# Optimization experiments

Measured on AMD Instinct MI355X. Metric: run time of the kernel, lower is better.

Reference implementation:

```python
import jax, jax.numpy as jnp
import numpy as np

WS = 7          # window size
NUM_HEADS = 12

def _relative_position_index(ws):
    # Same construction as the torch module; pure numpy constants.
    coords = np.stack(np.meshgrid(np.arange(ws), np.arange(ws), indexing='ij'))  # [2, ws, ws]
    flat = coords.reshape(2, -1)                                                 # [2, N]
    rel = flat[:, :, None] - flat[:, None, :]                                    # [2, N, N]
    rel = rel.transpose(1, 2, 0).copy()                                          # [N, N, 2]
    rel[:, :, 0] += ws - 1
    rel[:, :, 1] += ws - 1
    rel[:, :, 0] *= 2 * ws - 1
    return rel.sum(-1)                                                           # [N, N] int

REL_IDX = jnp.asarray(_relative_position_index(WS))

def setup_inputs() -> dict:
    key = jax.random.key(0)
    ks = jax.random.split(key, 7)
    C, H = 384, NUM_HEADS
    B_, N = 2048, WS * WS
    return {
        "x": jax.random.normal(ks[0], (B_, N, C), jnp.float32),
        "mask": jax.random.normal(ks[1], (64, N, N), jnp.float32),
        "qkv_w": jax.random.normal(ks[2], (3 * C, C), jnp.float32) * 0.02,
        "qkv_b": jax.random.normal(ks[3], (3 * C,), jnp.float32) * 0.02,
        "proj_w": jax.random.normal(ks[4], (C, C), jnp.float32) * 0.02,
        "proj_b": jax.random.normal(ks[5], (C,), jnp.float32) * 0.02,
        "rpb_table": jax.random.normal(ks[6], ((2 * WS - 1) ** 2, H), jnp.float32) * 0.02,
    }

def reference(x, mask, qkv_w, qkv_b, proj_w, proj_b, rpb_table):
    B_, N, C = x.shape
    H = NUM_HEADS
    hd = C // H
    scale = hd ** (-0.5)

    qkv = x @ qkv_w.T + qkv_b                                   # [B_, N, 3C]
    qkv = qkv.reshape(B_, N, 3, H, hd).transpose(2, 0, 3, 1, 4)  # [3, B_, H, N, hd]
    q, k, v = qkv[0], qkv[1], qkv[2]

    attn = jnp.einsum('bhnd,bhmd->bhnm', q * scale, k)          # [B_, H, N, N]

    bias = rpb_table[REL_IDX]                                   # [N, N, H]
    attn = attn + bias.transpose(2, 0, 1)[None]                 # + [1, H, N, N]

    nw = mask.shape[0]
    attn = attn.reshape(B_ // nw, nw, H, N, N) + mask[None, :, None]
    attn = attn.reshape(B_, H, N, N)
    attn = jax.nn.softmax(attn, axis=-1)

    out = jnp.einsum('bhnm,bhmd->bhnd', attn, v)                # [B_, H, N, hd]
    out = out.transpose(0, 2, 1, 3).reshape(B_, N, C)
    return out @ proj_w.T + proj_b
```

## Files before the change

kernel.cpp:

```cpp
#include <hip/hip_runtime.h>
#include <stdint.h>
#include <stddef.h>

#define BWIN 2048
#define NTOK 49
#define CDIM 384
#define HNUM 12
#define HD   32
#define MTOT (BWIN * NTOK)
#define SCALE 0.17677669529663687f

typedef __attribute__((ext_vector_type(8))) short short8;
typedef __attribute__((ext_vector_type(4))) float floatx4;

__device__ __forceinline__ unsigned short f2bf(float f) {
    union { float f; unsigned u; } v; v.f = f;
    unsigned u = v.u;
    u = u + 0x7fffu + ((u >> 16) & 1u);
    return (unsigned short)(u >> 16);
}
__device__ __forceinline__ float bf2f(unsigned short b) {
    union { unsigned u; float f; } v; v.u = ((unsigned)b) << 16;
    return v.f;
}

__device__ __forceinline__ void gload16(const void* g, void* l) {
    __builtin_amdgcn_global_load_lds(
        (const __attribute__((address_space(1))) void*)g,
        (__attribute__((address_space(3))) void*)l, 16, 0, 0);
}

#define XBLK  18816
#define WQBLK 216
#define WPBLK 72
__global__ __launch_bounds__(256) void convert_kernel(
    const float* __restrict__ x, const float* __restrict__ wq,
    const float* __restrict__ wp, unsigned short* __restrict__ xbf,
    unsigned short* __restrict__ wqbf, unsigned short* __restrict__ wpbf)
{
    int bid = blockIdx.x;
    const float* src; unsigned short* dst; size_t base;
    if (bid < XBLK)              { src = x;  dst = xbf;  base = (size_t)bid * 2048; }
    else if (bid < XBLK + WQBLK) { src = wq; dst = wqbf; base = (size_t)(bid - XBLK) * 2048; }
    else                         { src = wp; dst = wpbf; base = (size_t)(bid - XBLK - WQBLK) * 2048; }
    const size_t i = base + (size_t)threadIdx.x * 8;
    float4 a = *(const float4*)(src + i);
    float4 b = *(const float4*)(src + i + 4);
    unsigned short o[8] = {f2bf(a.x), f2bf(a.y), f2bf(a.z), f2bf(a.w),
                           f2bf(b.x), f2bf(b.y), f2bf(b.z), f2bf(b.w)};
    *(uint4*)(dst + i) = *(uint4*)o;
}

__global__ __launch_bounds__(256) void qkv_kernel(
    const unsigned short* __restrict__ a, const unsigned short* __restrict__ b,
    const float* __restrict__ bias, unsigned short* __restrict__ outq)
{
    __shared__ __align__(16) unsigned short lA[128 * 32];
    __shared__ __align__(16) unsigned short lB[128 * 32];

    const int tid = threadIdx.x;
    const int lane = tid & 63, w = tid >> 6;
    const int tN = blockIdx.x * 128;
    const int tM = blockIdx.y * 128;

    const int srow = (w << 5) + (lane >> 2);
    const int scol = (lane & 3) << 3;
    const unsigned short* gA = a + (size_t)(tM + srow) * CDIM + scol;
    const unsigned short* gB = b + (size_t)(tN + srow) * CDIM + scol;
    unsigned short* lAb = lA + (w << 10);
    unsigned short* lBb = lB + (w << 10);

    const int wm = (w & 1) << 6, wn = (w >> 1) << 6;
    const int cg = lane & 15, rg = lane >> 4;

    floatx4 acc[4][4];
    #pragma unroll
    for (int i = 0; i < 4; ++i)
        #pragma unroll
        for (int j = 0; j < 4; ++j) acc[i][j] = (floatx4){0.f, 0.f, 0.f, 0.f};

    for (int k0 = 0; k0 < CDIM; k0 += 32) {
        __syncthreads();
        gload16(gA + k0,              lAb);
        gload16(gA + k0 + 16 * CDIM,  lAb + 512);
        gload16(gB + k0,              lBb);
        gload16(gB + k0 + 16 * CDIM,  lBb + 512);
        __syncthreads();

        short8 af[4], bfr[4];
        #pragma unroll
        for (int i = 0; i < 4; ++i)
            af[i] = *(const short8*)&lA[(wm + 16 * i + cg) * 32 + rg * 8];
        #pragma unroll
        for (int j = 0; j < 4; ++j)
            bfr[j] = *(const short8*)&lB[(wn + 16 * j + cg) * 32 + rg * 8];
        #pragma unroll
        for (int i = 0; i < 4; ++i)
            #pragma unroll
            for (int j = 0; j < 4; ++j)
                acc[i][j] = __builtin_amdgcn_mfma_f32_16x16x32_bf16(af[i], bfr[j], acc[i][j], 0, 0, 0);
    }

    const int r0 = tM + wm + (rg << 2);
    #pragma unroll
    for (int j = 0; j < 4; ++j) {
        const int col = tN + wn + 16 * j + cg;
        const float bv = bias[col];
        const int which = col / CDIM;
        const int rem = col - which * CDIM;
        const int h = rem >> 5, d = rem & 31;
        #pragma unroll
        for (int i = 0; i < 4; ++i) {
            #pragma unroll
            for (int r = 0; r < 4; ++r) {
                const int row = r0 + 16 * i + r;
                const int bb = row / NTOK;
                const int n = row - bb * NTOK;
                const size_t oidx = ((((size_t)which * BWIN + bb) * HNUM + h) * NTOK + n) * HD + d;
                outq[oidx] = f2bf(acc[i][j][r] + bv);
            }
        }
    }
}

__global__ __launch_bounds__(256) void attn_kernel(
    const unsigned short* __restrict__ qkv, const float* __restrict__ mask,
    const float* __restrict__ rpb, unsigned short* __restrict__ outa)
{
    __shared__ __align__(16) unsigned short lq[64][40];
    __shared__ __align__(16) unsigned short lk[64][40];
    __shared__ __align__(16) unsigned short lvt[32][72];
    __shared__ __align__(16) unsigned short lp[64][72];

    const int b = blockIdx.x, h = blockIdx.y;
    const int tid = threadIdx.x;
    const size_t WHICH = (size_t)BWIN * HNUM * NTOK * HD;
    const size_t base = ((size_t)b * HNUM + h) * (NTOK * HD);

    for (int e = tid; e < 1152; e += 256)
        ((unsigned*)&lvt[0][0])[e] = 0u;
    if (tid < 240) {
        const int r = 49 + (tid >> 4), c = (tid & 15) * 2;
        *(unsigned*)&lq[r][c] = 0u;
        *(unsigned*)&lk[r][c] = 0u;
    }
    if (tid < 196) {
        const int n = tid >> 2, d = (tid & 3) * 8;
        *(uint4*)&lq[n][d] = *(const uint4*)(qkv + base + tid * 8);
        *(uint4*)&lk[n][d] = *(const uint4*)(qkv + base + WHICH + tid * 8);
    }
    __syncthreads();

    for (int e = tid; e < NTOK * HD; e += 256) {
        const int n = e >> 5, d = e & 31;
        lvt[d][n] = qkv[base + 2 * WHICH + e];
    }
    __syncthreads();

    const int w = tid >> 6, lane = tid & 63;
    const int cg = lane & 15;
    const int rg = lane >> 4;
    const int rbase = 16 * w + rg * 4;

    short8 aq = *(const short8*)&lq[16 * w + cg][rg * 8];
    floatx4 s[4];
    #pragma unroll
    for (int j = 0; j < 4; ++j) {
        short8 bk = *(const short8*)&lk[16 * j + cg][rg * 8];
        floatx4 z = {0, 0, 0, 0};
        s[j] = __builtin_amdgcn_mfma_f32_16x16x32_bf16(aq, bk, z, 0, 0, 0);
    }

    const float* mk = mask + (size_t)(b & 63) * (NTOK * NTOK);
    float vals[4][4];
    float m[4] = {-1e30f, -1e30f, -1e30f, -1e30f};
    #pragma unroll
    for (int j = 0; j < 4; ++j) {
        const int col = 16 * j + cg;
        const bool vc = col < NTOK;
        int yj = 0, xj = 0;
        if (vc) { yj = col / 7; xj = col - yj * 7; }
        #pragma unroll
        for (int r = 0; r < 4; ++r) {
            float v = -1e30f;
            if (vc) {
                const int row = rbase + r;
                const int rowc = row < NTOK ? row : NTOK - 1;
                const int yi = rowc / 7, xi = rowc - yi * 7;
                const int rel = (yi - yj + 6) * 13 + (xi - xj + 6);
                v = s[j][r] * SCALE + rpb[rel * HNUM + h] + mk[rowc * NTOK + col];
            }
            vals[j][r] = v;
            m[r] = fmaxf(m[r], v);
        }
    }
    #pragma unroll
    for (int st = 1; st < 16; st <<= 1) {
        #pragma unroll
        for (int r = 0; r < 4; ++r) m[r] = fmaxf(m[r], __shfl_xor(m[r], st));
    }
    float l[4] = {0.f, 0.f, 0.f, 0.f};
    #pragma unroll
    for (int j = 0; j < 4; ++j) {
        const int col = 16 * j + cg;
        #pragma unroll
        for (int r = 0; r < 4; ++r) {
            const float e = (col < NTOK) ? __expf(vals[j][r] - m[r]) : 0.f;
            l[r] += e;
            lp[rbase + r][col] = f2bf(e);
        }
    }
    #pragma unroll
    for (int st = 1; st < 16; st <<= 1) {
        #pragma unroll
        for (int r = 0; r < 4; ++r) l[r] += __shfl_xor(l[r], st);
    }
    float linv[4];
    #pragma unroll
    for (int r = 0; r < 4; ++r) linv[r] = 1.f / l[r];
    __syncthreads();

    #pragma unroll
    for (int n = 0; n < 2; ++n) {
        floatx4 o = {0, 0, 0, 0};
        #pragma unroll
        for (int kk = 0; kk < 2; ++kk) {
            short8 ap = *(const short8*)&lp[16 * w + cg][kk * 32 + rg * 8];
            short8 bv = *(const short8*)&lvt[16 * n + cg][kk * 32 + rg * 8];
            o = __builtin_amdgcn_mfma_f32_16x16x32_bf16(ap, bv, o, 0, 0, 0);
        }
        #pragma unroll
        for (int r = 0; r < 4; ++r) {
            const int row = rbase + r;
            if (row < NTOK)
                outa[((size_t)b * NTOK + row) * CDIM + h * HD + n * 16 + cg] =
                    f2bf(o[r] * linv[r]);
        }
    }
}

__global__ __launch_bounds__(256) void proj_kernel(
    const unsigned short* __restrict__ a, const unsigned short* __restrict__ b,
    const float* __restrict__ bias, float* __restrict__ out)
{
    __shared__ __align__(16) unsigned short lA[128 * 32];
    __shared__ __align__(16) unsigned short lB[128 * 32];

    const int tid = threadIdx.x;
    const int lane = tid & 63, w = tid >> 6;
    const int tN = blockIdx.x * 128;
    const int tM = blockIdx.y * 128;

    const int srow = (w << 5) + (lane >> 2);
    const int scol = (lane & 3) << 3;
    const unsigned short* gA = a + (size_t)(tM + srow) * CDIM + scol;
    const unsigned short* gB = b + (size_t)(tN + srow) * CDIM + scol;
    unsigned short* lAb = lA + (w << 10);
    unsigned short* lBb = lB + (w << 10);

    const int wm = (w & 1) << 6, wn = (w >> 1) << 6;
    const int cg = lane & 15, rg = lane >> 4;

    floatx4 acc[4][4];
    #pragma unroll
    for (int i = 0; i < 4; ++i)
        #pragma unroll
        for (int j = 0; j < 4; ++j) acc[i][j] = (floatx4){0.f, 0.f, 0.f, 0.f};

    for (int k0 = 0; k0 < CDIM; k0 += 32) {
        __syncthreads();
        gload16(gA + k0,             lAb);
        gload16(gA + k0 + 16 * CDIM, lAb + 512);
        gload16(gB + k0,             lBb);
        gload16(gB + k0 + 16 * CDIM, lBb + 512);
        __syncthreads();

        short8 af[4], bfr[4];
        #pragma unroll
        for (int i = 0; i < 4; ++i)
            af[i] = *(const short8*)&lA[(wm + 16 * i + cg) * 32 + rg * 8];
        #pragma unroll
        for (int j = 0; j < 4; ++j)
            bfr[j] = *(const short8*)&lB[(wn + 16 * j + cg) * 32 + rg * 8];
        #pragma unroll
        for (int i = 0; i < 4; ++i)
            #pragma unroll
            for (int j = 0; j < 4; ++j)
                acc[i][j] = __builtin_amdgcn_mfma_f32_16x16x32_bf16(af[i], bfr[j], acc[i][j], 0, 0, 0);
    }

    const int r0 = tM + wm + (rg << 2);
    #pragma unroll
    for (int j = 0; j < 4; ++j) {
        const int col = tN + wn + 16 * j + cg;
        const float bv = bias[col];
        #pragma unroll
        for (int i = 0; i < 4; ++i) {
            #pragma unroll
            for (int r = 0; r < 4; ++r) {
                const int row = r0 + 16 * i + r;
                out[(size_t)row * CDIM + col] = acc[i][j][r] + bv;
            }
        }
    }
}

extern "C" void kernel_launch(void* const* d_in, const int* in_sizes, int n_in,
                              void* d_out, int out_size, void* d_ws, size_t ws_size,
                              hipStream_t stream) {
    const float* x      = (const float*)d_in[0];
    const float* mask   = (const float*)d_in[1];
    const float* qkv_w  = (const float*)d_in[2];
    const float* qkv_b  = (const float*)d_in[3];
    const float* proj_w = (const float*)d_in[4];
    const float* proj_b = (const float*)d_in[5];
    const float* rpb    = (const float*)d_in[6];
    float* out = (float*)d_out;

    unsigned short* ws_qkv  = (unsigned short*)d_ws;
    unsigned short* xbf     = ws_qkv + (size_t)3 * BWIN * HNUM * NTOK * HD;
    unsigned short* ws_attn = xbf;
    unsigned short* wqbf    = xbf + (size_t)MTOT * CDIM;
    unsigned short* wpbf    = wqbf + (size_t)3 * CDIM * CDIM;

    convert_kernel<<<XBLK + WQBLK + WPBLK, 256, 0, stream>>>(x, qkv_w, proj_w, xbf, wqbf, wpbf);
    qkv_kernel<<<dim3(1152 / 128, MTOT / 128), 256, 0, stream>>>(xbf, wqbf, qkv_b, ws_qkv);
    attn_kernel<<<dim3(BWIN, HNUM), 256, 0, stream>>>(ws_qkv, mask, rpb, ws_attn);
    proj_kernel<<<dim3(CDIM / 128, MTOT / 128), 256, 0, stream>>>(ws_attn, wpbf, proj_b, out);
}
```

Baseline: 704.8 us.

## Precompute fused mask+position bias, fold scale into Q, drop softmax max pass

A new kernel precomputes the combined relative-position bias and window mask, scaled by log2(e), for each window and head. It stores the result in the MFMA accumulator fragment layout, so the attention kernel loads it as the initial accumulator of the QK^T MFMA. The softmax scale times log2(e) is folded into Q in the QKV epilogue, and the row-max reduction is removed, so the probabilities come from exp2f of the scores directly. V is now loaded with one vectorized read per thread and transposed from registers, which also drops one barrier. Without the max subtraction, exp2f can overflow if scores grow large, and the extra bias buffer adds workspace use and one more launch.

```diff
diff --git a/kernel.cpp b/kernel.cpp
--- a/kernel.cpp
+++ b/kernel.cpp
@@ -8,7 +8,8 @@
 #define HNUM 12
 #define HD   32
 #define MTOT (BWIN * NTOK)
-#define SCALE 0.17677669529663687f
+#define LOG2E 1.4426950408889634f
+#define QSCALE ((float)(0.17677669529663687 * 1.4426950408889634))
 
 typedef __attribute__((ext_vector_type(8))) short short8;
 typedef __attribute__((ext_vector_type(4))) float floatx4;
@@ -18,10 +19,6 @@
     unsigned u = v.u;
     u = u + 0x7fffu + ((u >> 16) & 1u);
     return (unsigned short)(u >> 16);
-}
-__device__ __forceinline__ float bf2f(unsigned short b) {
-    union { unsigned u; float f; } v; v.u = ((unsigned)b) << 16;
-    return v.f;
 }
 
 __device__ __forceinline__ void gload16(const void* g, void* l) {
@@ -51,6 +48,41 @@
     *(uint4*)(dst + i) = *(uint4*)o;
 }
 
+__global__ __launch_bounds__(256) void bias_kernel(
+    const float* __restrict__ mask, const float* __restrict__ rpb,
+    float* __restrict__ cb)
+{
+    const int bm = blockIdx.x, h = blockIdx.y;
+    const int tid = threadIdx.x;
+    const int w = tid >> 6, lane = tid & 63;
+    const int cg = lane & 15, rg = lane >> 4;
+    const int rbase = 16 * w + (rg << 2);
+    const float* mk = mask + (size_t)bm * (NTOK * NTOK);
+    float o[16];
+    #pragma unroll
+    for (int j = 0; j < 4; ++j) {
+        const int col = 16 * j + cg;
+        const bool vc = col < NTOK;
+        int yj = 0, xj = 0;
+        if (vc) { yj = col / 7; xj = col - yj * 7; }
+        #pragma unroll
+        for (int r = 0; r < 4; ++r) {
+            const int row = rbase + r;
+            float v = -1e30f;
+            if (vc && row < NTOK) {
+                const int yi = row / 7, xi = row - yi * 7;
+                const int rel = (yi - yj + 6) * 13 + (xi - xj + 6);
+                v = (rpb[rel * HNUM + h] + mk[row * NTOK + col]) * LOG2E;
+            }
+            o[4 * j + r] = v;
+        }
+    }
+    float* dst = cb + ((size_t)bm * HNUM + h) * 4096 + (size_t)tid * 16;
+    #pragma unroll
+    for (int j = 0; j < 4; ++j)
+        *(float4*)(dst + 4 * j) = *(const float4*)(o + 4 * j);
+}
+
 __global__ __launch_bounds__(256) void qkv_kernel(
     const unsigned short* __restrict__ a, const unsigned short* __restrict__ b,
     const float* __restrict__ bias, unsigned short* __restrict__ outq)
@@ -109,6 +141,7 @@
         const int which = col / CDIM;
         const int rem = col - which * CDIM;
         const int h = rem >> 5, d = rem & 31;
+        const float sc = (which == 0) ? QSCALE : 1.0f;
         #pragma unroll
         for (int i = 0; i < 4; ++i) {
             #pragma unroll
@@ -117,15 +150,15 @@
                 const int bb = row / NTOK;
                 const int n = row - bb * NTOK;
                 const size_t oidx = ((((size_t)which * BWIN + bb) * HNUM + h) * NTOK + n) * HD + d;
-                outq[oidx] = f2bf(acc[i][j][r] + bv);
+                outq[oidx] = f2bf((acc[i][j][r] + bv) * sc);
             }
         }
     }
 }
 
 __global__ __launch_bounds__(256) void attn_kernel(
-    const unsigned short* __restrict__ qkv, const float* __restrict__ mask,
-    const float* __restrict__ rpb, unsigned short* __restrict__ outa)
+    const unsigned short* __restrict__ qkv, const float* __restrict__ cb,
+    unsigned short* __restrict__ outa)
 {
     __shared__ __align__(16) unsigned short lq[64][40];
     __shared__ __align__(16) unsigned short lk[64][40];
@@ -136,6 +169,11 @@
     const int tid = threadIdx.x;
     const size_t WHICH = (size_t)BWIN * HNUM * NTOK * HD;
     const size_t base = ((size_t)b * HNUM + h) * (NTOK * HD);
+
+    const float* cbp = cb + ((size_t)(b & 63) * HNUM + h) * 4096 + (size_t)tid * 16;
+    floatx4 z[4];
+    #pragma unroll
+    for (int j = 0; j < 4; ++j) z[j] = *(const floatx4*)(cbp + 4 * j);
 
     for (int e = tid; e < 1152; e += 256)
         ((unsigned*)&lvt[0][0])[e] = 0u;
@@ -144,18 +182,22 @@
         *(unsigned*)&lq[r][c] = 0u;
         *(unsigned*)&lk[r][c] = 0u;
     }
+    uint4 vreg;
     if (tid < 196) {
         const int n = tid >> 2, d = (tid & 3) * 8;
         *(uint4*)&lq[n][d] = *(const uint4*)(qkv + base + tid * 8);
         *(uint4*)&lk[n][d] = *(const uint4*)(qkv + base + WHICH + tid * 8);
+        vreg = *(const uint4*)(qkv + base + 2 * WHICH + tid * 8);
     }
     __syncthreads();
 
-    for (int e = tid; e < NTOK * HD; e += 256) {
-        const int n = e >> 5, d = e & 31;
-        lvt[d][n] = qkv[base + 2 * WHICH + e];
-    }
-    __syncthreads();
+    if (tid < 196) {
+        const int n = tid >> 2, d0 = (tid & 3) * 8;
+        const unsigned short* vp = (const unsigned short*)&vreg;
+        #pragma unroll
+        for (int jj = 0; jj < 8; ++jj)
+            lvt[d0 + jj][n] = vp[jj];
+    }
 
     const int w = tid >> 6, lane = tid & 63;
     const int cg = lane & 15;
@@ -167,45 +209,16 @@
     #pragma unroll
     for (int j = 0; j < 4; ++j) {
         short8 bk = *(const short8*)&lk[16 * j + cg][rg * 8];
-        floatx4 z = {0, 0, 0, 0};
-        s[j] = __builtin_amdgcn_mfma_f32_16x16x32_bf16(aq, bk, z, 0, 0, 0);
-    }
-
-    const float* mk = mask + (size_t)(b & 63) * (NTOK * NTOK);
-    float vals[4][4];
-    float m[4] = {-1e30f, -1e30f, -1e30f, -1e30f};
+        s[j] = __builtin_amdgcn_mfma_f32_16x16x32_bf16(aq, bk, z[j], 0, 0, 0);
+    }
+
+    float l[4] = {0.f, 0.f, 0.f, 0.f};
     #pragma unroll
     for (int j = 0; j < 4; ++j) {
         const int col = 16 * j + cg;
-        const bool vc = col < NTOK;
-        int yj = 0, xj = 0;
-        if (vc) { yj = col / 7; xj = col - yj * 7; }
         #pragma unroll
         for (int r = 0; r < 4; ++r) {
-            float v = -1e30f;
-            if (vc) {
-                const int row = rbase + r;
-                const int rowc = row < NTOK ? row : NTOK - 1;
-                const int yi = rowc / 7, xi = rowc - yi * 7;
-                const int rel = (yi - yj + 6) * 13 + (xi - xj + 6);
-                v = s[j][r] * SCALE + rpb[rel * HNUM + h] + mk[rowc * NTOK + col];
-            }
-            vals[j][r] = v;
-            m[r] = fmaxf(m[r], v);
-        }
-    }
-    #pragma unroll
-    for (int st = 1; st < 16; st <<= 1) {
-        #pragma unroll
-        for (int r = 0; r < 4; ++r) m[r] = fmaxf(m[r], __shfl_xor(m[r], st));
-    }
-    float l[4] = {0.f, 0.f, 0.f, 0.f};
-    #pragma unroll
-    for (int j = 0; j < 4; ++j) {
-        const int col = 16 * j + cg;
-        #pragma unroll
-        for (int r = 0; r < 4; ++r) {
-            const float e = (col < NTOK) ? __expf(vals[j][r] - m[r]) : 0.f;
+            const float e = exp2f(s[j][r]);
             l[r] += e;
             lp[rbase + r][col] = f2bf(e);
         }
@@ -322,9 +335,11 @@
     unsigned short* ws_attn = xbf;
     unsigned short* wqbf    = xbf + (size_t)MTOT * CDIM;
     unsigned short* wpbf    = wqbf + (size_t)3 * CDIM * CDIM;
+    float* cbias            = (float*)(wpbf + (size_t)CDIM * CDIM);
 
     convert_kernel<<<XBLK + WQBLK + WPBLK, 256, 0, stream>>>(x, qkv_w, proj_w, xbf, wqbf, wpbf);
+    bias_kernel<<<dim3(64, HNUM), 256, 0, stream>>>(mask, rpb, cbias);
     qkv_kernel<<<dim3(1152 / 128, MTOT / 128), 256, 0, stream>>>(xbf, wqbf, qkv_b, ws_qkv);
-    attn_kernel<<<dim3(BWIN, HNUM), 256, 0, stream>>>(ws_qkv, mask, rpb, ws_attn);
+    attn_kernel<<<dim3(BWIN, HNUM), 256, 0, stream>>>(ws_qkv, cbias, ws_attn);
     proj_kernel<<<dim3(CDIM / 128, MTOT / 128), 256, 0, stream>>>(ws_attn, wpbf, proj_b, out);
 }
```

Result: faster. 624.2 us (-11.4%).
